# Performance work log

Measured on AMD Instinct MI355X. Metric: run time of the kernel, lower is better.

## Reference

```python
import jax, jax.numpy as jnp
import numpy as np

B, C_IN, C_OUT = 2, 32, 32
N_IN = 128 * 128            # input grid points
N_OUT = 128 * 128           # output grid points
KERNEL_SIZE = 9             # (3-1)*4 + 1 for kernel_shape=[3,4], piecewise_linear basis
NNZ = 1_500_000             # sparse entries in psi (kernel_size, n_out, n_in)


def setup_inputs() -> dict:
    key = jax.random.key(0)
    ks = jax.random.split(key, 8)
    scale = (1.0 / C_IN) ** 0.5  # sqrt(1/groupsize), groups=1
    return {
        "x": jax.random.normal(ks[0], (B, C_IN, N_IN), jnp.float32),
        "quadrature_weights": jax.random.uniform(ks[1], (N_IN,), jnp.float32, 0.5, 1.5) / N_IN,
        "psi_vals": jax.random.uniform(ks[2], (NNZ,), jnp.float32),
        "weight": scale * jax.random.normal(ks[3], (C_OUT, C_IN, KERNEL_SIZE), jnp.float32),
        "bias": jnp.zeros((C_OUT,), jnp.float32),
        "psi_idx_k": jax.random.randint(ks[4], (NNZ,), 0, KERNEL_SIZE, dtype=jnp.int32),
        "psi_idx_out": jax.random.randint(ks[5], (NNZ,), 0, N_OUT, dtype=jnp.int32),
        "psi_idx_in": jax.random.randint(ks[6], (NNZ,), 0, N_IN, dtype=jnp.int32),
        "n_out": N_OUT,
    }


def reference(x, quadrature_weights, psi_vals, weight, bias,
              psi_idx_k, psi_idx_out, psi_idx_in, n_out):
    # x: (B, C, n_in); weight: (O, C, K); psi is sparse (K, n_out, n_in)
    Bb, C, n_in = x.shape
    K = weight.shape[2]
    # pre-multiply by quadrature weights, layout (n_in, B, C) for gather
    xq = (x * quadrature_weights[None, None, :]).transpose(2, 0, 1)
    # gather-weight: contribution of each sparse entry  -> (nnz, B, C)
    contrib = xq[psi_idx_in] * psi_vals[:, None, None]
    # scatter-add into (kernel, out) bins == sparse psi @ xq
    seg = psi_idx_k * n_out + psi_idx_out
    xk = jax.ops.segment_sum(contrib, seg, num_segments=K * n_out)
    xk = xk.reshape(K, n_out, Bb, C)  # (K, n_out, B, C)
    # channel/kernel mixing with learned weight (groups=1)
    out = jnp.einsum("knbc,ock->bon", xk, weight) + bias[None, :, None]
    return out  # (B, out_channels, n_out)
```

## Files before the change

### kernel.cpp

```cpp
#include <hip/hip_runtime.h>

#define N_IN   16384
#define N_OUT  16384
#define KSZ    9
#define CIN    32
#define COUT   32
#define BC     64
#define NCB    256
#define CHA    4096
#define ECAP_A 8192
#define ROWS   144
#define XSTR   68
#define SCAP   2048

union PrepSH {
    struct { int cnt[NCB]; int cntE[NCB]; int gbase[NCB]; int cursor[NCB];
             float2 slist[CHA]; } bin;
    struct { float tile[64 * 65]; } xqp;
};

__global__ __launch_bounds__(512) void k_prep(
        const float* __restrict__ x, const float* __restrict__ qw,
        const float* __restrict__ vals, const float* __restrict__ w,
        const int* __restrict__ ik, const int* __restrict__ io,
        const int* __restrict__ ii, float* __restrict__ xq,
        float2* __restrict__ sivA, int* __restrict__ gcntA,
        float* __restrict__ wT, int nnz, int nchA) {
    __shared__ PrepSH sh;
    const int t = threadIdx.x;
    const int bid = blockIdx.x;

    if (bid >= nchA) {
        if (bid < nchA + 256) {
            const int in0 = (bid - nchA) * 64;
#pragma unroll
            for (int i = 0; i < 8; ++i) {
                int idx = t + i * 512;
                int bcl = idx >> 6, inl = idx & 63;
                sh.xqp.tile[bcl * 65 + inl] = x[bcl * N_IN + in0 + inl];
            }
            __syncthreads();
#pragma unroll
            for (int i = 0; i < 8; ++i) {
                int idx = t + i * 512;
                int inl = idx >> 6, bcl = idx & 63;
                xq[(size_t)(in0 + inl) * BC + bcl] = sh.xqp.tile[bcl * 65 + inl] * qw[in0 + inl];
            }
        } else {
            for (int i = t; i < COUT * CIN * KSZ; i += 512) {
                int o = i / (CIN * KSZ);
                int r = i - o * (CIN * KSZ);
                int c = r / KSZ;
                int k = r - c * KSZ;
                wT[((k * 8 + (o >> 2)) * 32 + c) * 4 + (o & 3)] = w[i];
            }
        }
        return;
    }

    if (t < NCB) sh.bin.cnt[t] = 0;
    __syncthreads();
    const int base = bid * CHA;
    const int e0   = base + t * 8;

    float vv[8]; int pk[8]; int bk[8]; bool hv[8];
    if (e0 + 8 <= nnz) {
        int4 a0 = *(const int4*)(io + e0),  a1 = *(const int4*)(io + e0 + 4);
        int4 b0 = *(const int4*)(ii + e0),  b1 = *(const int4*)(ii + e0 + 4);
        int4 k0 = *(const int4*)(ik + e0),  k1 = *(const int4*)(ik + e0 + 4);
        float4 d0 = *(const float4*)(vals + e0), d1 = *(const float4*)(vals + e0 + 4);
        int ov[8] = {a0.x, a0.y, a0.z, a0.w, a1.x, a1.y, a1.z, a1.w};
        int iv[8] = {b0.x, b0.y, b0.z, b0.w, b1.x, b1.y, b1.z, b1.w};
        int kv[8] = {k0.x, k0.y, k0.z, k0.w, k1.x, k1.y, k1.z, k1.w};
        float dv[8] = {d0.x, d0.y, d0.z, d0.w, d1.x, d1.y, d1.z, d1.w};
#pragma unroll
        for (int j = 0; j < 8; ++j) {
            hv[j] = true;
            bk[j] = ov[j] >> 6;
            pk[j] = (int)(((unsigned)(ov[j] >> 4) << 22)) | (iv[j] << 8) | (kv[j] * 16 + (ov[j] & 15));
            vv[j] = dv[j];
        }
    } else {
#pragma unroll
        for (int j = 0; j < 8; ++j) {
            int e = e0 + j;
            hv[j] = (e < nnz);
            if (hv[j]) {
                int o = io[e];
                bk[j] = o >> 6;
                pk[j] = (int)(((unsigned)(o >> 4) << 22)) | (ii[e] << 8) | (ik[e] * 16 + (o & 15));
                vv[j] = vals[e];
            } else { bk[j] = 0; pk[j] = 0; vv[j] = 0.f; }
        }
    }
#pragma unroll
    for (int j = 0; j < 8; ++j) if (hv[j]) atomicAdd(&sh.bin.cnt[bk[j]], 1);
    __syncthreads();
    if (t < NCB) {
        int cv = sh.bin.cnt[t];
        sh.bin.gbase[t] = t * ECAP_A + (cv ? atomicAdd(&gcntA[t], cv) : 0);
    }
    if (t < 64) {
        int carry = 0;
#pragma unroll
        for (int seg = 0; seg < 4; ++seg) {
            int idx = seg * 64 + t;
            int v = sh.bin.cnt[idx];
            int orig = v;
#pragma unroll
            for (int off = 1; off < 64; off <<= 1) {
                int u = __shfl_up(v, off);
                if (t >= off) v += u;
            }
            sh.bin.cntE[idx]   = carry + v - orig;
            sh.bin.cursor[idx] = carry + v - orig;
            carry += __shfl(v, 63);
        }
    }
    __syncthreads();
#pragma unroll
    for (int j = 0; j < 8; ++j) {
        if (hv[j]) {
            int pos = atomicAdd(&sh.bin.cursor[bk[j]], 1);
            sh.bin.slist[pos] = make_float2(vv[j], __int_as_float(pk[j]));
        }
    }
    __syncthreads();
    const int m = min(nnz - base, CHA);
    for (int p = t; p < m; p += 512) {
        float2 f2 = sh.bin.slist[p];
        int cb = (int)((unsigned)__float_as_int(f2.y) >> 24);
        int dest = sh.bin.gbase[cb] + (p - sh.bin.cntE[cb]);
        if (dest < (cb + 1) * ECAP_A) sivA[dest] = f2;
    }
}

__global__ __launch_bounds__(512) void k_fused6(const float* __restrict__ xq,
        const float2* __restrict__ sivA, const int* __restrict__ gcntA,
        const float* __restrict__ wT, const float* __restrict__ bias,
        float* __restrict__ out) {
    __shared__ __align__(16) float sxk[80 * XSTR];
    __shared__ float2 slist[SCAP];
    __shared__ int    rowStart[ROWS + 1];
    __shared__ int    cursor[ROWS];
    __shared__ int    mcur;
    const int tid  = threadIdx.x;
    const int lane = tid & 63;
    const int wv   = __builtin_amdgcn_readfirstlane(tid >> 6);
    const unsigned f = blockIdx.x;

    if (tid < ROWS) rowStart[tid] = 0;
    if (tid == 0) mcur = 0;
    __syncthreads();

    const int cb = (int)(f >> 2);
    const int mA = min(gcntA[cb], ECAP_A);
    const float2* src = sivA + (size_t)cb * ECAP_A;
    float2* tmp = (float2*)sxk;
    for (int i = tid; i < mA; i += 512) {
        float2 v = src[i];
        unsigned fid = (unsigned)__float_as_int(v.y) >> 22;
        if (fid == f) {
            int pos = atomicAdd(&mcur, 1);
            if (pos < SCAP) {
                tmp[pos] = v;
                atomicAdd(&rowStart[__float_as_int(v.y) & 0xFF], 1);
            }
        }
    }
    __syncthreads();
    const int m2 = min(mcur, SCAP);
    if (wv == 0) {
        int carry = 0;
#pragma unroll
        for (int i0 = 0; i0 < 192; i0 += 64) {
            int idx = i0 + lane;
            int v = (idx < ROWS) ? rowStart[idx] : 0;
            int orig = v;
#pragma unroll
            for (int off = 1; off < 64; off <<= 1) {
                int u = __shfl_up(v, off);
                if (lane >= off) v += u;
            }
            if (idx < ROWS) {
                int excl = carry + v - orig;
                rowStart[idx] = excl;
                cursor[idx]   = excl;
            }
            carry += __shfl(v, 63);
        }
        if (lane == 0) rowStart[ROWS] = carry;
    }
    __syncthreads();
    for (int i = tid; i < m2; i += 512) {
        float2 v = tmp[i];
        int p = __float_as_int(v.y);
        int pos = atomicAdd(&cursor[p & 0xFF], 1);
        slist[pos] = make_float2(v.x, __int_as_float(p & 0x3FFF00));
    }
    __syncthreads();

    const char* xqb   = (const char*)xq;
    const int   lane4 = lane * 4;
    const int   h     = lane >> 4;
    const int   nl    = lane & 15;
    float acc[4] = {0.f, 0.f, 0.f, 0.f};

#pragma unroll
    for (int ph = 0; ph < 2; ++ph) {
        const int rbase = ph ? 80 : 0;
        const int rend  = ph ? 144 : 80;
        const int nrows = rend - rbase;
        for (int i = tid; i < nrows * XSTR; i += 512) sxk[i] = 0.f;
        __syncthreads();
        for (int r = rbase + wv; r < rend; r += 8) {
            const int a = rowStart[r], b = rowStart[r + 1];
            if (a >= b) continue;
            float acc0 = 0.f, acc1 = 0.f, acc2 = 0.f, acc3 = 0.f;
            int i = a;
            for (; i + 7 < b; i += 8) {
                float2 v0 = slist[i],     v1 = slist[i + 1], v2 = slist[i + 2], v3 = slist[i + 3];
                float2 v4 = slist[i + 4], v5 = slist[i + 5], v6 = slist[i + 6], v7 = slist[i + 7];
                acc0 += *(const float*)(xqb + (__float_as_int(v0.y) + lane4)) * v0.x;
                acc1 += *(const float*)(xqb + (__float_as_int(v1.y) + lane4)) * v1.x;
                acc2 += *(const float*)(xqb + (__float_as_int(v2.y) + lane4)) * v2.x;
                acc3 += *(const float*)(xqb + (__float_as_int(v3.y) + lane4)) * v3.x;
                acc0 += *(const float*)(xqb + (__float_as_int(v4.y) + lane4)) * v4.x;
                acc1 += *(const float*)(xqb + (__float_as_int(v5.y) + lane4)) * v5.x;
                acc2 += *(const float*)(xqb + (__float_as_int(v6.y) + lane4)) * v6.x;
                acc3 += *(const float*)(xqb + (__float_as_int(v7.y) + lane4)) * v7.x;
            }
            for (; i + 3 < b; i += 4) {
                float2 v0 = slist[i], v1 = slist[i + 1], v2 = slist[i + 2], v3 = slist[i + 3];
                acc0 += *(const float*)(xqb + (__float_as_int(v0.y) + lane4)) * v0.x;
                acc1 += *(const float*)(xqb + (__float_as_int(v1.y) + lane4)) * v1.x;
                acc2 += *(const float*)(xqb + (__float_as_int(v2.y) + lane4)) * v2.x;
                acc3 += *(const float*)(xqb + (__float_as_int(v3.y) + lane4)) * v3.x;
            }
            for (; i < b; ++i) {
                float2 v = slist[i];
                acc0 += *(const float*)(xqb + (__float_as_int(v.y) + lane4)) * v.x;
            }
            sxk[(r - rbase) * XSTR + lane] = (acc0 + acc1) + (acc2 + acc3);
        }
        __syncthreads();
        if (lane < 32) {
            const int kbase = ph ? 5 : 0;
            const int kcnt  = ph ? 4 : 5;
            for (int kk = 0; kk < kcnt; ++kk) {
                const float* xr = &sxk[(kk * 16 + nl) * XSTR + h * 32];
                const float* wp = &wT[((kbase + kk) * 8 + wv) * 128];
#pragma unroll
                for (int c4 = 0; c4 < 8; ++c4) {
                    float4 xv = *(const float4*)&xr[c4 * 4];
#pragma unroll
                    for (int cc = 0; cc < 4; ++cc) {
                        float xval = (&xv.x)[cc];
#pragma unroll
                        for (int j = 0; j < 4; ++j)
                            acc[j] += xval * wp[(c4 * 4 + cc) * 4 + j];
                    }
                }
            }
        }
        __syncthreads();
    }

    if (lane < 32) {
        const int n0 = (int)f * 16;
#pragma unroll
        for (int j = 0; j < 4; ++j) {
            int o = wv * 4 + j;
            out[((size_t)h * COUT + o) * N_OUT + n0 + nl] = acc[j] + bias[o];
        }
    }
}

extern "C" void kernel_launch(void* const* d_in, const int* in_sizes, int n_in,
                              void* d_out, int out_size, void* d_ws, size_t ws_size,
                              hipStream_t stream) {
    const float* x    = (const float*)d_in[0];
    const float* qw   = (const float*)d_in[1];
    const float* vals = (const float*)d_in[2];
    const float* w    = (const float*)d_in[3];
    const float* bias = (const float*)d_in[4];
    const int*   ik   = (const int*)d_in[5];
    const int*   io   = (const int*)d_in[6];
    const int*   ii   = (const int*)d_in[7];
    const int    nnz  = in_sizes[2];
    const int    nchA = (nnz + CHA - 1) / CHA;

    char* ws = (char*)d_ws;
    float*  xq    = (float*)ws;  ws += (size_t)N_IN * BC * 4;
    float2* sivA  = (float2*)ws; ws += (size_t)NCB * ECAP_A * 8;
    int*    gcntA = (int*)ws;    ws += NCB * 4;
    float*  wT    = (float*)ws;  ws += (size_t)COUT * CIN * KSZ * 4;

    hipMemsetAsync(gcntA, 0, NCB * sizeof(int), stream);
    k_prep  <<<nchA + 257, 512, 0, stream>>>(x, qw, vals, w, ik, io, ii,
                                             xq, sivA, gcntA, wT, nnz, nchA);
    k_fused6<<<1024, 512, 0, stream>>>(xq, sivA, gcntA, wT, bias, (float*)d_out);
}
```

Baseline: 147.4 us.

## Fuse prep and compute kernels into one persistent kernel with grid barrier

Merges the binning/transpose prep kernel and the gather-mix kernel into one 1024-block kernel. The two phases are separated by a software grid-wide barrier built on an atomic counter, which is zeroed alongside gcntA. This removes the second kernel launch and the gap between dependent launches. It also replaces the per-element shared atomic in the match-filter step with wave ballot compaction. The barrier relies on all 1024 blocks being co-resident (launch_bounds 512,8 and the LDS union size); if they are not, the kernel deadlocks.

```diff
diff --git a/kernel.cpp b/kernel.cpp
--- a/kernel.cpp
+++ b/kernel.cpp
@@ -12,170 +12,178 @@
 #define ROWS   144
 #define XSTR   68
 #define SCAP   2048
-
-union PrepSH {
+#define GRID   1024
+
+union SH {
     struct { int cnt[NCB]; int cntE[NCB]; int gbase[NCB]; int cursor[NCB];
              float2 slist[CHA]; } bin;
     struct { float tile[64 * 65]; } xqp;
+    struct { __align__(16) float sxk[80 * XSTR]; float2 slist[SCAP];
+             int rowStart[ROWS + 1]; int cursor[ROWS]; int mcur; } fu;
 };
 
-__global__ __launch_bounds__(512) void k_prep(
+__global__ __launch_bounds__(512, 8) void k_all(
         const float* __restrict__ x, const float* __restrict__ qw,
         const float* __restrict__ vals, const float* __restrict__ w,
-        const int* __restrict__ ik, const int* __restrict__ io,
-        const int* __restrict__ ii, float* __restrict__ xq,
-        float2* __restrict__ sivA, int* __restrict__ gcntA,
-        float* __restrict__ wT, int nnz, int nchA) {
-    __shared__ PrepSH sh;
-    const int t = threadIdx.x;
-    const int bid = blockIdx.x;
-
-    if (bid >= nchA) {
-        if (bid < nchA + 256) {
-            const int in0 = (bid - nchA) * 64;
-#pragma unroll
-            for (int i = 0; i < 8; ++i) {
-                int idx = t + i * 512;
-                int bcl = idx >> 6, inl = idx & 63;
-                sh.xqp.tile[bcl * 65 + inl] = x[bcl * N_IN + in0 + inl];
-            }
-            __syncthreads();
-#pragma unroll
-            for (int i = 0; i < 8; ++i) {
-                int idx = t + i * 512;
-                int inl = idx >> 6, bcl = idx & 63;
-                xq[(size_t)(in0 + inl) * BC + bcl] = sh.xqp.tile[bcl * 65 + inl] * qw[in0 + inl];
-            }
-        } else {
-            for (int i = t; i < COUT * CIN * KSZ; i += 512) {
-                int o = i / (CIN * KSZ);
-                int r = i - o * (CIN * KSZ);
-                int c = r / KSZ;
-                int k = r - c * KSZ;
-                wT[((k * 8 + (o >> 2)) * 32 + c) * 4 + (o & 3)] = w[i];
-            }
-        }
-        return;
-    }
-
-    if (t < NCB) sh.bin.cnt[t] = 0;
-    __syncthreads();
-    const int base = bid * CHA;
-    const int e0   = base + t * 8;
-
-    float vv[8]; int pk[8]; int bk[8]; bool hv[8];
-    if (e0 + 8 <= nnz) {
-        int4 a0 = *(const int4*)(io + e0),  a1 = *(const int4*)(io + e0 + 4);
-        int4 b0 = *(const int4*)(ii + e0),  b1 = *(const int4*)(ii + e0 + 4);
-        int4 k0 = *(const int4*)(ik + e0),  k1 = *(const int4*)(ik + e0 + 4);
-        float4 d0 = *(const float4*)(vals + e0), d1 = *(const float4*)(vals + e0 + 4);
-        int ov[8] = {a0.x, a0.y, a0.z, a0.w, a1.x, a1.y, a1.z, a1.w};
-        int iv[8] = {b0.x, b0.y, b0.z, b0.w, b1.x, b1.y, b1.z, b1.w};
-        int kv[8] = {k0.x, k0.y, k0.z, k0.w, k1.x, k1.y, k1.z, k1.w};
-        float dv[8] = {d0.x, d0.y, d0.z, d0.w, d1.x, d1.y, d1.z, d1.w};
-#pragma unroll
-        for (int j = 0; j < 8; ++j) {
-            hv[j] = true;
-            bk[j] = ov[j] >> 6;
-            pk[j] = (int)(((unsigned)(ov[j] >> 4) << 22)) | (iv[j] << 8) | (kv[j] * 16 + (ov[j] & 15));
-            vv[j] = dv[j];
-        }
-    } else {
-#pragma unroll
-        for (int j = 0; j < 8; ++j) {
-            int e = e0 + j;
-            hv[j] = (e < nnz);
-            if (hv[j]) {
-                int o = io[e];
-                bk[j] = o >> 6;
-                pk[j] = (int)(((unsigned)(o >> 4) << 22)) | (ii[e] << 8) | (ik[e] * 16 + (o & 15));
-                vv[j] = vals[e];
-            } else { bk[j] = 0; pk[j] = 0; vv[j] = 0.f; }
-        }
-    }
-#pragma unroll
-    for (int j = 0; j < 8; ++j) if (hv[j]) atomicAdd(&sh.bin.cnt[bk[j]], 1);
-    __syncthreads();
-    if (t < NCB) {
-        int cv = sh.bin.cnt[t];
-        sh.bin.gbase[t] = t * ECAP_A + (cv ? atomicAdd(&gcntA[t], cv) : 0);
-    }
-    if (t < 64) {
-        int carry = 0;
-#pragma unroll
-        for (int seg = 0; seg < 4; ++seg) {
-            int idx = seg * 64 + t;
-            int v = sh.bin.cnt[idx];
-            int orig = v;
-#pragma unroll
-            for (int off = 1; off < 64; off <<= 1) {
-                int u = __shfl_up(v, off);
-                if (t >= off) v += u;
-            }
-            sh.bin.cntE[idx]   = carry + v - orig;
-            sh.bin.cursor[idx] = carry + v - orig;
-            carry += __shfl(v, 63);
-        }
-    }
-    __syncthreads();
-#pragma unroll
-    for (int j = 0; j < 8; ++j) {
-        if (hv[j]) {
-            int pos = atomicAdd(&sh.bin.cursor[bk[j]], 1);
-            sh.bin.slist[pos] = make_float2(vv[j], __int_as_float(pk[j]));
-        }
-    }
-    __syncthreads();
-    const int m = min(nnz - base, CHA);
-    for (int p = t; p < m; p += 512) {
-        float2 f2 = sh.bin.slist[p];
-        int cb = (int)((unsigned)__float_as_int(f2.y) >> 24);
-        int dest = sh.bin.gbase[cb] + (p - sh.bin.cntE[cb]);
-        if (dest < (cb + 1) * ECAP_A) sivA[dest] = f2;
-    }
-}
-
-__global__ __launch_bounds__(512) void k_fused6(const float* __restrict__ xq,
-        const float2* __restrict__ sivA, const int* __restrict__ gcntA,
-        const float* __restrict__ wT, const float* __restrict__ bias,
-        float* __restrict__ out) {
-    __shared__ __align__(16) float sxk[80 * XSTR];
-    __shared__ float2 slist[SCAP];
-    __shared__ int    rowStart[ROWS + 1];
-    __shared__ int    cursor[ROWS];
-    __shared__ int    mcur;
+        const float* __restrict__ bias, const int* __restrict__ ik,
+        const int* __restrict__ io, const int* __restrict__ ii,
+        float* __restrict__ xq, float2* __restrict__ sivA,
+        int* __restrict__ gcntA, int* __restrict__ done,
+        float* __restrict__ wT, float* __restrict__ out, int nnz, int nchA) {
+    __shared__ SH sh;
     const int tid  = threadIdx.x;
     const int lane = tid & 63;
     const int wv   = __builtin_amdgcn_readfirstlane(tid >> 6);
-    const unsigned f = blockIdx.x;
-
-    if (tid < ROWS) rowStart[tid] = 0;
-    if (tid == 0) mcur = 0;
+    const int bid  = blockIdx.x;
+
+    if (bid < nchA) {
+        if (tid < NCB) sh.bin.cnt[tid] = 0;
+        __syncthreads();
+        const int base = bid * CHA;
+        const int e0   = base + tid * 8;
+        float vv[8]; int pk[8]; int bk[8]; bool hv[8];
+        if (e0 + 8 <= nnz) {
+            int4 a0 = *(const int4*)(io + e0),  a1 = *(const int4*)(io + e0 + 4);
+            int4 b0 = *(const int4*)(ii + e0),  b1 = *(const int4*)(ii + e0 + 4);
+            int4 k0 = *(const int4*)(ik + e0),  k1 = *(const int4*)(ik + e0 + 4);
+            float4 d0 = *(const float4*)(vals + e0), d1 = *(const float4*)(vals + e0 + 4);
+            int ov[8] = {a0.x, a0.y, a0.z, a0.w, a1.x, a1.y, a1.z, a1.w};
+            int iv[8] = {b0.x, b0.y, b0.z, b0.w, b1.x, b1.y, b1.z, b1.w};
+            int kv[8] = {k0.x, k0.y, k0.z, k0.w, k1.x, k1.y, k1.z, k1.w};
+            float dv[8] = {d0.x, d0.y, d0.z, d0.w, d1.x, d1.y, d1.z, d1.w};
+#pragma unroll
+            for (int j = 0; j < 8; ++j) {
+                hv[j] = true;
+                bk[j] = ov[j] >> 6;
+                pk[j] = (int)(((unsigned)(ov[j] >> 4) << 22)) | (iv[j] << 8) | (kv[j] * 16 + (ov[j] & 15));
+                vv[j] = dv[j];
+            }
+        } else {
+#pragma unroll
+            for (int j = 0; j < 8; ++j) {
+                int e = e0 + j;
+                hv[j] = (e < nnz);
+                if (hv[j]) {
+                    int o = io[e];
+                    bk[j] = o >> 6;
+                    pk[j] = (int)(((unsigned)(o >> 4) << 22)) | (ii[e] << 8) | (ik[e] * 16 + (o & 15));
+                    vv[j] = vals[e];
+                } else { bk[j] = 0; pk[j] = 0; vv[j] = 0.f; }
+            }
+        }
+#pragma unroll
+        for (int j = 0; j < 8; ++j) if (hv[j]) atomicAdd(&sh.bin.cnt[bk[j]], 1);
+        __syncthreads();
+        if (tid < NCB) {
+            int cv = sh.bin.cnt[tid];
+            sh.bin.gbase[tid] = tid * ECAP_A + (cv ? atomicAdd(&gcntA[tid], cv) : 0);
+        }
+        if (tid < 64) {
+            int carry = 0;
+#pragma unroll
+            for (int seg = 0; seg < 4; ++seg) {
+                int idx = seg * 64 + tid;
+                int v = sh.bin.cnt[idx];
+                int orig = v;
+#pragma unroll
+                for (int off = 1; off < 64; off <<= 1) {
+                    int u = __shfl_up(v, off);
+                    if (tid >= off) v += u;
+                }
+                sh.bin.cntE[idx]   = carry + v - orig;
+                sh.bin.cursor[idx] = carry + v - orig;
+                carry += __shfl(v, 63);
+            }
+        }
+        __syncthreads();
+#pragma unroll
+        for (int j = 0; j < 8; ++j) {
+            if (hv[j]) {
+                int pos = atomicAdd(&sh.bin.cursor[bk[j]], 1);
+                sh.bin.slist[pos] = make_float2(vv[j], __int_as_float(pk[j]));
+            }
+        }
+        __syncthreads();
+        const int m = min(nnz - base, CHA);
+        for (int p = tid; p < m; p += 512) {
+            float2 f2 = sh.bin.slist[p];
+            int cb = (int)((unsigned)__float_as_int(f2.y) >> 24);
+            int dest = sh.bin.gbase[cb] + (p - sh.bin.cntE[cb]);
+            if (dest < (cb + 1) * ECAP_A) sivA[dest] = f2;
+        }
+    } else if (bid < nchA + 256) {
+        const int in0 = (bid - nchA) * 64;
+#pragma unroll
+        for (int i = 0; i < 8; ++i) {
+            int idx = tid + i * 512;
+            int bcl = idx >> 6, inl = idx & 63;
+            sh.xqp.tile[bcl * 65 + inl] = x[bcl * N_IN + in0 + inl];
+        }
+        __syncthreads();
+#pragma unroll
+        for (int i = 0; i < 8; ++i) {
+            int idx = tid + i * 512;
+            int inl = idx >> 6, bcl = idx & 63;
+            xq[(size_t)(in0 + inl) * BC + bcl] = sh.xqp.tile[bcl * 65 + inl] * qw[in0 + inl];
+        }
+    } else if (bid == nchA + 256) {
+        for (int i = tid; i < COUT * CIN * KSZ; i += 512) {
+            int o = i / (CIN * KSZ);
+            int r = i - o * (CIN * KSZ);
+            int c = r / KSZ;
+            int k = r - c * KSZ;
+            wT[((k * 8 + (o >> 2)) * 32 + c) * 4 + (o & 3)] = w[i];
+        }
+    }
+
+    __syncthreads();
+    if (tid == 0) {
+        __threadfence();
+        atomicAdd(done, 1);
+        while (atomicAdd(done, 0) < GRID) __builtin_amdgcn_s_sleep(8);
+    }
+    __syncthreads();
+    __threadfence();
+
+    const unsigned f = (unsigned)bid;
+    if (tid < ROWS) sh.fu.rowStart[tid] = 0;
+    if (tid == 0) sh.fu.mcur = 0;
     __syncthreads();
 
     const int cb = (int)(f >> 2);
     const int mA = min(gcntA[cb], ECAP_A);
     const float2* src = sivA + (size_t)cb * ECAP_A;
-    float2* tmp = (float2*)sxk;
-    for (int i = tid; i < mA; i += 512) {
-        float2 v = src[i];
-        unsigned fid = (unsigned)__float_as_int(v.y) >> 22;
-        if (fid == f) {
-            int pos = atomicAdd(&mcur, 1);
-            if (pos < SCAP) {
-                tmp[pos] = v;
-                atomicAdd(&rowStart[__float_as_int(v.y) & 0xFF], 1);
-            }
-        }
-    }
-    __syncthreads();
-    const int m2 = min(mcur, SCAP);
+    float2* tmp = (float2*)sh.fu.sxk;
+    const int iters = (mA + 511) >> 9;
+    for (int it = 0; it < iters; ++it) {
+        int i = (it << 9) + tid;
+        bool inr = (i < mA);
+        float2 v = inr ? src[i] : make_float2(0.f, __int_as_float(-1));
+        bool match = inr && (((unsigned)__float_as_int(v.y) >> 22) == f);
+        unsigned long long mask = __ballot(match);
+        if (mask) {
+            int ldr    = (int)(__ffsll((unsigned long long)mask) - 1);
+            int prefix = __popcll(mask & ((1ULL << lane) - 1ULL));
+            int base2  = 0;
+            if (lane == ldr) base2 = atomicAdd(&sh.fu.mcur, __popcll(mask));
+            base2 = __shfl(base2, ldr);
+            if (match) {
+                int pos = base2 + prefix;
+                if (pos < SCAP) {
+                    tmp[pos] = v;
+                    atomicAdd(&sh.fu.rowStart[__float_as_int(v.y) & 0xFF], 1);
+                }
+            }
+        }
+    }
+    __syncthreads();
+    const int m2 = min(sh.fu.mcur, SCAP);
     if (wv == 0) {
         int carry = 0;
 #pragma unroll
         for (int i0 = 0; i0 < 192; i0 += 64) {
             int idx = i0 + lane;
-            int v = (idx < ROWS) ? rowStart[idx] : 0;
+            int v = (idx < ROWS) ? sh.fu.rowStart[idx] : 0;
             int orig = v;
 #pragma unroll
             for (int off = 1; off < 64; off <<= 1) {
@@ -184,19 +192,19 @@
             }
             if (idx < ROWS) {
                 int excl = carry + v - orig;
-                rowStart[idx] = excl;
-                cursor[idx]   = excl;
+                sh.fu.rowStart[idx] = excl;
+                sh.fu.cursor[idx]   = excl;
             }
             carry += __shfl(v, 63);
         }
-        if (lane == 0) rowStart[ROWS] = carry;
+        if (lane == 0) sh.fu.rowStart[ROWS] = carry;
     }
     __syncthreads();
     for (int i = tid; i < m2; i += 512) {
         float2 v = tmp[i];
         int p = __float_as_int(v.y);
-        int pos = atomicAdd(&cursor[p & 0xFF], 1);
-        slist[pos] = make_float2(v.x, __int_as_float(p & 0x3FFF00));
+        int pos = atomicAdd(&sh.fu.cursor[p & 0xFF], 1);
+        sh.fu.slist[pos] = make_float2(v.x, __int_as_float(p & 0x3FFF00));
     }
     __syncthreads();
 
@@ -211,16 +219,18 @@
         const int rbase = ph ? 80 : 0;
         const int rend  = ph ? 144 : 80;
         const int nrows = rend - rbase;
-        for (int i = tid; i < nrows * XSTR; i += 512) sxk[i] = 0.f;
+        for (int i = tid; i < nrows * XSTR; i += 512) sh.fu.sxk[i] = 0.f;
         __syncthreads();
         for (int r = rbase + wv; r < rend; r += 8) {
-            const int a = rowStart[r], b = rowStart[r + 1];
+            const int a = sh.fu.rowStart[r], b = sh.fu.rowStart[r + 1];
             if (a >= b) continue;
             float acc0 = 0.f, acc1 = 0.f, acc2 = 0.f, acc3 = 0.f;
             int i = a;
             for (; i + 7 < b; i += 8) {
-                float2 v0 = slist[i],     v1 = slist[i + 1], v2 = slist[i + 2], v3 = slist[i + 3];
-                float2 v4 = slist[i + 4], v5 = slist[i + 5], v6 = slist[i + 6], v7 = slist[i + 7];
+                float2 v0 = sh.fu.slist[i],     v1 = sh.fu.slist[i + 1];
+                float2 v2 = sh.fu.slist[i + 2], v3 = sh.fu.slist[i + 3];
+                float2 v4 = sh.fu.slist[i + 4], v5 = sh.fu.slist[i + 5];
+                float2 v6 = sh.fu.slist[i + 6], v7 = sh.fu.slist[i + 7];
                 acc0 += *(const float*)(xqb + (__float_as_int(v0.y) + lane4)) * v0.x;
                 acc1 += *(const float*)(xqb + (__float_as_int(v1.y) + lane4)) * v1.x;
                 acc2 += *(const float*)(xqb + (__float_as_int(v2.y) + lane4)) * v2.x;
@@ -231,24 +241,25 @@
                 acc3 += *(const float*)(xqb + (__float_as_int(v7.y) + lane4)) * v7.x;
             }
             for (; i + 3 < b; i += 4) {
-                float2 v0 = slist[i], v1 = slist[i + 1], v2 = slist[i + 2], v3 = slist[i + 3];
+                float2 v0 = sh.fu.slist[i],     v1 = sh.fu.slist[i + 1];
+                float2 v2 = sh.fu.slist[i + 2], v3 = sh.fu.slist[i + 3];
                 acc0 += *(const float*)(xqb + (__float_as_int(v0.y) + lane4)) * v0.x;
                 acc1 += *(const float*)(xqb + (__float_as_int(v1.y) + lane4)) * v1.x;
                 acc2 += *(const float*)(xqb + (__float_as_int(v2.y) + lane4)) * v2.x;
                 acc3 += *(const float*)(xqb + (__float_as_int(v3.y) + lane4)) * v3.x;
             }
             for (; i < b; ++i) {
-                float2 v = slist[i];
+                float2 v = sh.fu.slist[i];
                 acc0 += *(const float*)(xqb + (__float_as_int(v.y) + lane4)) * v.x;
             }
-            sxk[(r - rbase) * XSTR + lane] = (acc0 + acc1) + (acc2 + acc3);
+            sh.fu.sxk[(r - rbase) * XSTR + lane] = (acc0 + acc1) + (acc2 + acc3);
         }
         __syncthreads();
         if (lane < 32) {
             const int kbase = ph ? 5 : 0;
             const int kcnt  = ph ? 4 : 5;
             for (int kk = 0; kk < kcnt; ++kk) {
-                const float* xr = &sxk[(kk * 16 + nl) * XSTR + h * 32];
+                const float* xr = &sh.fu.sxk[(kk * 16 + nl) * XSTR + h * 32];
                 const float* wp = &wT[((kbase + kk) * 8 + wv) * 128];
 #pragma unroll
                 for (int c4 = 0; c4 < 8; ++c4) {
@@ -294,10 +305,11 @@
     float*  xq    = (float*)ws;  ws += (size_t)N_IN * BC * 4;
     float2* sivA  = (float2*)ws; ws += (size_t)NCB * ECAP_A * 8;
     int*    gcntA = (int*)ws;    ws += NCB * 4;
+    int*    done  = (int*)ws;    ws += 4;
     float*  wT    = (float*)ws;  ws += (size_t)COUT * CIN * KSZ * 4;
 
-    hipMemsetAsync(gcntA, 0, NCB * sizeof(int), stream);
-    k_prep  <<<nchA + 257, 512, 0, stream>>>(x, qw, vals, w, ik, io, ii,
-                                             xq, sivA, gcntA, wT, nnz, nchA);
-    k_fused6<<<1024, 512, 0, stream>>>(xq, sivA, gcntA, wT, bias, (float*)d_out);
+    hipMemsetAsync(gcntA, 0, (NCB + 1) * sizeof(int), stream);
+    k_all<<<GRID, 512, 0, stream>>>(x, qw, vals, w, bias, ik, io, ii,
+                                    xq, sivA, gcntA, done, wT,
+                                    (float*)d_out, nnz, nchA);
 }
```

New measurement: 434.1 us. 2.94x slower.
